# Kernel tuning notes

Hardware: AMD Instinct MI355X
Metric: run time of the kernel (lower is better)

Reference implementation:

```python
import jax, jax.numpy as jnp
import numpy as np

H = 512
NHALF = 32  # N // 2 complex conjugate pairs
LLEN = 8192


def setup_inputs() -> dict:
    key = jax.random.key(0)
    k1, k2, k3 = jax.random.split(key, 3)
    # log_dt ~ uniform in [log(dt_min), log(dt_max)]
    log_dt = jax.random.uniform(k1, (H,), dtype=jnp.float32) * (
        np.log(0.1) - np.log(0.001)) + np.log(0.001)
    # C: complex randn stored as (H, NHALF, 2) real view
    C = jax.random.normal(k2, (H, NHALF, 2), dtype=jnp.float32)
    log_A_real = jnp.log(0.5 * jnp.ones((H, NHALF), dtype=jnp.float32))
    A_imag = np.pi * jnp.broadcast_to(
        jnp.arange(NHALF, dtype=jnp.float32), (H, NHALF))
    return {"C": C, "log_dt": log_dt, "log_A_real": log_A_real,
            "A_imag": A_imag, "L": LLEN}


def reference(C, log_dt, log_A_real, A_imag, L):
    # zoh discretization of diagonal SSM -> kernel K of shape (H, L)
    dt = jnp.exp(log_dt)                                  # (H,)
    Cc = (C[..., 0] + 1j * C[..., 1]).astype(jnp.complex64)  # (H, n)
    A = (-jnp.exp(log_A_real) + 1j * A_imag).astype(jnp.complex64)  # (H, n)
    dtA = A * dt[:, None]                                 # (H, n)
    t = jnp.arange(L, dtype=jnp.float32)                  # (L,)
    C_scaled = Cc * (jnp.exp(dtA) - 1.0) / A              # (H, n)
    # Vandermonde: exp(dtA)^t over length L, reduce over n
    T = jnp.exp(dtA[:, :, None] * t[None, None, :])       # (H, n, L) complex
    K = 2.0 * jnp.einsum('hn,hnl->hl', C_scaled, T).real  # (H, L)
    return K
```

## Files before the change

kernel.cpp:

```cpp
#include <hip/hip_runtime.h>
#include <math.h>

#define HDIM   512
#define NH     32
#define LLEN   8192
#define BLOCK  256
#define LSPLIT 2
#define LPB    (LLEN / LSPLIT)
#define JSTEPS (LPB / (BLOCK * 4))

__global__ __launch_bounds__(BLOCK) void s4d_kernel(
    const float* __restrict__ C,
    const float* __restrict__ log_dt,
    const float* __restrict__ log_A_real,
    const float* __restrict__ A_imag,
    float* __restrict__ out)
{
    __shared__ float  s_cre[NH], s_cim[NH];
    __shared__ float  s_w1r[NH], s_w1i[NH];
    __shared__ float  s_Wr[NH],  s_Wi[NH];
    __shared__ float  s_dre[NH];
    __shared__ double s_dim[NH];

    const int h   = blockIdx.y;
    const int ls  = blockIdx.x;
    const int tid = threadIdx.x;

    if (tid < NH) {
        const int n = tid;
        const double TWO_PI = 6.283185307179586476925287;
        const double dt  = exp((double)log_dt[h]);
        const double Are = -exp((double)log_A_real[h * NH + n]);
        const double Aim = (double)A_imag[h * NH + n];
        const double dre = Are * dt, dim = Aim * dt;

        double es, ec;
        sincos(dim, &es, &ec);
        const double em  = exp(dre);
        const double nre = em * ec - 1.0, nim = em * es;
        const double den = Are * Are + Aim * Aim;
        const double fre = (nre * Are + nim * Aim) / den;
        const double fim = (nim * Are - nre * Aim) / den;
        const double Cre = (double)C[(h * NH + n) * 2 + 0];
        const double Cim = (double)C[(h * NH + n) * 2 + 1];
        s_cre[n] = (float)(2.0 * (Cre * fre - Cim * fim));
        s_cim[n] = (float)(2.0 * (Cre * fim + Cim * fre));

        s_w1r[n] = (float)(em * ec);
        s_w1i[n] = (float)(em * es);

        double r = dim * 1024.0 * (1.0 / TWO_PI);
        r -= floor(r);
        double ss, cc;
        sincos(r * TWO_PI, &ss, &cc);
        const double m = exp(dre * 1024.0);
        s_Wr[n] = (float)(m * cc);
        s_Wi[n] = (float)(m * ss);

        s_dre[n] = (float)dre;
        s_dim[n] = dim;
    }
    __syncthreads();

    const int lbase = ls * LPB + 4 * tid;
    const float flbase = (float)lbase;

    float acc[JSTEPS][4];
#pragma unroll
    for (int j = 0; j < JSTEPS; ++j)
#pragma unroll
        for (int k = 0; k < 4; ++k) acc[j][k] = 0.0f;

#pragma unroll 1
    for (int n = 0; n < NH; ++n) {
        const float cr = s_cre[n], ci = s_cim[n];
        const float w1r = s_w1r[n], w1i = s_w1i[n];
        const float Wr = s_Wr[n],  Wi = s_Wi[n];

        const double TWO_PI = 6.283185307179586476925287;
        double r = s_dim[n] * (double)lbase * (1.0 / TWO_PI);
        r -= floor(r);
        float s, c;
        __sincosf((float)(r * TWO_PI), &s, &c);
        const float mag = __expf(s_dre[n] * flbase);

        float Tr[4], Ti[4];
        Tr[0] = mag * c;
        Ti[0] = mag * s;
#pragma unroll
        for (int k = 1; k < 4; ++k) {
            Tr[k] = fmaf(Tr[k-1], w1r, -Ti[k-1] * w1i);
            Ti[k] = fmaf(Tr[k-1], w1i,  Ti[k-1] * w1r);
        }

#pragma unroll
        for (int j = 0; j < JSTEPS; ++j) {
#pragma unroll
            for (int k = 0; k < 4; ++k)
                acc[j][k] = fmaf(cr, Tr[k], fmaf(-ci, Ti[k], acc[j][k]));
            if (j < JSTEPS - 1) {
#pragma unroll
                for (int k = 0; k < 4; ++k) {
                    const float nTr = fmaf(Tr[k], Wr, -Ti[k] * Wi);
                    const float nTi = fmaf(Tr[k], Wi,  Ti[k] * Wr);
                    Tr[k] = nTr; Ti[k] = nTi;
                }
            }
        }
    }

    float* orow = out + (size_t)h * LLEN;
#pragma unroll
    for (int j = 0; j < JSTEPS; ++j) {
        float4 v = make_float4(acc[j][0], acc[j][1], acc[j][2], acc[j][3]);
        *(float4*)(orow + lbase + j * (BLOCK * 4)) = v;
    }
}

extern "C" void kernel_launch(void* const* d_in, const int* in_sizes, int n_in,
                              void* d_out, int out_size, void* d_ws, size_t ws_size,
                              hipStream_t stream) {
    const float* C          = (const float*)d_in[0];
    const float* log_dt     = (const float*)d_in[1];
    const float* log_A_real = (const float*)d_in[2];
    const float* A_imag     = (const float*)d_in[3];
    float* out = (float*)d_out;

    dim3 grid(LSPLIT, HDIM);
    s4d_kernel<<<grid, BLOCK, 0, stream>>>(C, log_dt, log_A_real, A_imag, out);
}
```

Before: 84.38 us.

## Use table-factored powers and second-order real recurrence for Vandermonde sum

Replaces the per-thread double-precision range reduction and sincos/exp of z^l with two small shared tables (z^(16i) and block-offset z^(256j)) whose product gives each thread's starting power. The taken real part is then propagated along 16 contiguous outputs per thread using the second-order recurrence y_{l+1} = 2Re(z) y_l - |z|^2 y_{l-1}, cutting the complex multiply work to about two FMAs per output per mode. Table setup now uses all threads in double precision, and two modes are processed per iteration. The risk is error growth over the 16-step real recurrence and float table products, and the per-thread store pattern changes to 16 contiguous floats.

```diff
diff --git a/kernel.cpp b/kernel.cpp
--- a/kernel.cpp
+++ b/kernel.cpp
@@ -7,7 +7,7 @@
 #define BLOCK  256
 #define LSPLIT 2
 #define LPB    (LLEN / LSPLIT)
-#define JSTEPS (LPB / (BLOCK * 4))
+#define LPT    16
 
 __global__ __launch_bounds__(BLOCK) void s4d_kernel(
     const float* __restrict__ C,
@@ -16,104 +16,109 @@
     const float* __restrict__ A_imag,
     float* __restrict__ out)
 {
-    __shared__ float  s_cre[NH], s_cim[NH];
-    __shared__ float  s_w1r[NH], s_w1i[NH];
-    __shared__ float  s_Wr[NH],  s_Wi[NH];
-    __shared__ float  s_dre[NH];
-    __shared__ double s_dim[NH];
+    __shared__ float2 tabA[NH][16];
+    __shared__ float2 tabB[NH][16];
+    __shared__ float4 s_cw[NH];
+    __shared__ float2 s_pq[NH];
 
     const int h   = blockIdx.y;
     const int ls  = blockIdx.x;
     const int tid = threadIdx.x;
 
-    if (tid < NH) {
-        const int n = tid;
-        const double TWO_PI = 6.283185307179586476925287;
+    {
+        const int n = tid & 31;
+        const int g = tid >> 5;
         const double dt  = exp((double)log_dt[h]);
         const double Are = -exp((double)log_A_real[h * NH + n]);
         const double Aim = (double)A_imag[h * NH + n];
         const double dre = Are * dt, dim = Aim * dt;
 
-        double es, ec;
-        sincos(dim, &es, &ec);
-        const double em  = exp(dre);
-        const double nre = em * ec - 1.0, nim = em * es;
-        const double den = Are * Are + Aim * Aim;
-        const double fre = (nre * Are + nim * Aim) / den;
-        const double fim = (nim * Are - nre * Aim) / den;
-        const double Cre = (double)C[(h * NH + n) * 2 + 0];
-        const double Cim = (double)C[(h * NH + n) * 2 + 1];
-        s_cre[n] = (float)(2.0 * (Cre * fre - Cim * fim));
-        s_cim[n] = (float)(2.0 * (Cre * fim + Cim * fre));
+        const bool   isB  = (g >= 4);
+        const int    i0   = (isB ? (g - 4) : g) * 4;
+        const double step = isB ? 256.0 : 16.0;
+        const double base = isB ? ((double)(LPB * ls) + 256.0 * (double)i0)
+                                : (16.0 * (double)i0);
 
-        s_w1r[n] = (float)(em * ec);
-        s_w1i[n] = (float)(em * es);
+        double s0, c0; sincos(dim * base, &s0, &c0);
+        const double m0 = exp(dre * base);
+        double er = m0 * c0, ei = m0 * s0;
+        double ss, cs; sincos(dim * step, &ss, &cs);
+        const double ms = exp(dre * step);
+        const double str = ms * cs, sti = ms * ss;
 
-        double r = dim * 1024.0 * (1.0 / TWO_PI);
-        r -= floor(r);
-        double ss, cc;
-        sincos(r * TWO_PI, &ss, &cc);
-        const double m = exp(dre * 1024.0);
-        s_Wr[n] = (float)(m * cc);
-        s_Wi[n] = (float)(m * ss);
+        float2* dst = isB ? &tabB[n][0] : &tabA[n][0];
+        for (int k = 0; k < 4; ++k) {
+            dst[i0 + k] = make_float2((float)er, (float)ei);
+            const double t = er * str - ei * sti;
+            ei = er * sti + ei * str;
+            er = t;
+        }
 
-        s_dre[n] = (float)dre;
-        s_dim[n] = dim;
+        if (g == 0) {
+            double s1, c1; sincos(dim, &s1, &c1);
+            const double em  = exp(dre);
+            const double w1r = em * c1, w1i = em * s1;
+            const double nre = w1r - 1.0, nim = w1i;
+            const double den = Are * Are + Aim * Aim;
+            const double fre = (nre * Are + nim * Aim) / den;
+            const double fim = (nim * Are - nre * Aim) / den;
+            const double Cre = (double)C[(h * NH + n) * 2 + 0];
+            const double Cim = (double)C[(h * NH + n) * 2 + 1];
+            s_cw[n] = make_float4((float)(2.0 * (Cre * fre - Cim * fim)),
+                                  (float)(2.0 * (Cre * fim + Cim * fre)),
+                                  (float)w1r, (float)w1i);
+            s_pq[n] = make_float2((float)(2.0 * w1r), (float)(em * em));
+        }
     }
     __syncthreads();
 
-    const int lbase = ls * LPB + 4 * tid;
-    const float flbase = (float)lbase;
+    const int lo = tid & 15, hi = tid >> 4;
 
-    float acc[JSTEPS][4];
+    float acc[LPT];
 #pragma unroll
-    for (int j = 0; j < JSTEPS; ++j)
-#pragma unroll
-        for (int k = 0; k < 4; ++k) acc[j][k] = 0.0f;
+    for (int l = 0; l < LPT; ++l) acc[l] = 0.0f;
 
 #pragma unroll 1
-    for (int n = 0; n < NH; ++n) {
-        const float cr = s_cre[n], ci = s_cim[n];
-        const float w1r = s_w1r[n], w1i = s_w1i[n];
-        const float Wr = s_Wr[n],  Wi = s_Wi[n];
+    for (int n = 0; n < NH; n += 2) {
+        const float2 Aa = tabA[n][lo],     Ba = tabB[n][hi];
+        const float2 Ab = tabA[n + 1][lo], Bb = tabB[n + 1][hi];
+        const float4 cwa = s_cw[n], cwb = s_cw[n + 1];
+        const float2 pqa = s_pq[n], pqb = s_pq[n + 1];
 
-        const double TWO_PI = 6.283185307179586476925287;
-        double r = s_dim[n] * (double)lbase * (1.0 / TWO_PI);
-        r -= floor(r);
-        float s, c;
-        __sincosf((float)(r * TWO_PI), &s, &c);
-        const float mag = __expf(s_dre[n] * flbase);
+        const float Tar = fmaf(Aa.x, Ba.x, -(Aa.y * Ba.y));
+        const float Tai = fmaf(Aa.x, Ba.y,   Aa.y * Ba.x);
+        const float Tbr = fmaf(Ab.x, Bb.x, -(Ab.y * Bb.y));
+        const float Tbi = fmaf(Ab.x, Bb.y,   Ab.y * Bb.x);
 
-        float Tr[4], Ti[4];
-        Tr[0] = mag * c;
-        Ti[0] = mag * s;
-#pragma unroll
-        for (int k = 1; k < 4; ++k) {
-            Tr[k] = fmaf(Tr[k-1], w1r, -Ti[k-1] * w1i);
-            Ti[k] = fmaf(Tr[k-1], w1i,  Ti[k-1] * w1r);
-        }
+        float ypa = fmaf(cwa.x, Tar, -(cwa.y * Tai));
+        float ypb = fmaf(cwb.x, Tbr, -(cwb.y * Tbi));
+
+        const float T1ar = fmaf(Tar, cwa.z, -(Tai * cwa.w));
+        const float T1ai = fmaf(Tar, cwa.w,   Tai * cwa.z);
+        const float T1br = fmaf(Tbr, cwb.z, -(Tbi * cwb.w));
+        const float T1bi = fmaf(Tbr, cwb.w,   Tbi * cwb.z);
+
+        float ya = fmaf(cwa.x, T1ar, -(cwa.y * T1ai));
+        float yb = fmaf(cwb.x, T1br, -(cwb.y * T1bi));
+
+        acc[0] += ypa + ypb;
+        acc[1] += ya  + yb;
 
 #pragma unroll
-        for (int j = 0; j < JSTEPS; ++j) {
-#pragma unroll
-            for (int k = 0; k < 4; ++k)
-                acc[j][k] = fmaf(cr, Tr[k], fmaf(-ci, Ti[k], acc[j][k]));
-            if (j < JSTEPS - 1) {
-#pragma unroll
-                for (int k = 0; k < 4; ++k) {
-                    const float nTr = fmaf(Tr[k], Wr, -Ti[k] * Wi);
-                    const float nTi = fmaf(Tr[k], Wi,  Ti[k] * Wr);
-                    Tr[k] = nTr; Ti[k] = nTi;
-                }
-            }
+        for (int l = 2; l < LPT; ++l) {
+            const float za = fmaf(pqa.x, ya, -(pqa.y * ypa));
+            const float zb = fmaf(pqb.x, yb, -(pqb.y * ypb));
+            acc[l] += za + zb;
+            ypa = ya; ya = za;
+            ypb = yb; yb = zb;
         }
     }
 
-    float* orow = out + (size_t)h * LLEN;
+    float* orow = out + (size_t)h * LLEN + ls * LPB + LPT * tid;
 #pragma unroll
-    for (int j = 0; j < JSTEPS; ++j) {
-        float4 v = make_float4(acc[j][0], acc[j][1], acc[j][2], acc[j][3]);
-        *(float4*)(orow + lbase + j * (BLOCK * 4)) = v;
+    for (int j = 0; j < 4; ++j) {
+        *(float4*)(orow + 4 * j) =
+            make_float4(acc[4*j], acc[4*j+1], acc[4*j+2], acc[4*j+3]);
     }
 }
 
```

New measurement: 80.98 us. 4.0% less time.
